# Kernel optimization log

Hardware: AMD Instinct MI355X
Metric: run time of the kernel (lower is better)

Reference implementation:

```python
import jax, jax.numpy as jnp
import numpy as np

DIM = 1024
NUM_HEADS = 16
HD = DIM // NUM_HEADS  # 64
ROPE_DIM = 64
ROPE_BASE = 10000.0


def setup_inputs() -> dict:
    key = jax.random.key(0)
    ks = jax.random.split(key, 5)
    B, N = 2, 2048
    s = 0.02
    return {
        "x": jax.random.normal(ks[0], (B, N, DIM), dtype=jnp.float32),
        "qkv_w": jax.random.normal(ks[1], (3 * DIM, DIM), dtype=jnp.float32) * s,
        "qkv_b": jax.random.normal(ks[2], (3 * DIM,), dtype=jnp.float32) * s,
        "proj_w": jax.random.normal(ks[3], (DIM, DIM), dtype=jnp.float32) * s,
        "proj_b": jax.random.normal(ks[4], (DIM,), dtype=jnp.float32) * s,
    }


def _apply_rope(t):
    # t: [B, H, N, D] with D even; interleaved (even, odd) pair rotation
    D = t.shape[-1]
    N = t.shape[2]
    pos = jnp.arange(N, dtype=t.dtype)
    inv = 1.0 / (ROPE_BASE ** (jnp.arange(0, D, 2, dtype=t.dtype) / D))
    freqs = pos[:, None] * inv[None, :]          # [N, D/2]
    cos = jnp.cos(freqs)[None, None]             # [1,1,N,D/2]
    sin = jnp.sin(freqs)[None, None]
    e = t[..., 0::2]
    o = t[..., 1::2]
    eo = e * cos - o * sin
    oo = e * sin + o * cos
    return jnp.stack([eo, oo], axis=-1).reshape(t.shape)


def reference(x, qkv_w, qkv_b, proj_w, proj_b):
    B, N, C = x.shape
    H, D = NUM_HEADS, HD
    scale = D ** -0.5
    qkv = x @ qkv_w.T + qkv_b                     # [B,N,3C]
    qkv = qkv.reshape(B, N, 3, H, D).transpose(2, 0, 3, 1, 4)  # [3,B,H,N,D]
    q, k, v = qkv[0], qkv[1], qkv[2]
    # RoPE on first ROPE_DIM dims of each head (here ROPE_DIM == HD)
    q = jnp.concatenate([_apply_rope(q[..., :ROPE_DIM]), q[..., ROPE_DIM:]], axis=-1)
    k = jnp.concatenate([_apply_rope(k[..., :ROPE_DIM]), k[..., ROPE_DIM:]], axis=-1)
    attn = jnp.einsum('bhnd,bhmd->bhnm', q, k) * scale
    attn = jax.nn.softmax(attn, axis=-1)
    out = jnp.einsum('bhnm,bhmd->bhnd', attn, v)  # [B,H,N,D]
    out = out.transpose(0, 2, 1, 3).reshape(B, N, C)
    return out @ proj_w.T + proj_b
```

## Files before the change

### kernel.cpp

```cpp
#include <hip/hip_runtime.h>
#include <hip/hip_bf16.h>
#include <stdint.h>

#define DIM   1024
#define NH    16
#define HDIM  64
#define SEQ   2048
#define BATCH 2
#define BHN   32
#define MTOK  4096
#define SC2   0.18033688f

using u16 = unsigned short;
using u32 = unsigned int;
typedef __attribute__((ext_vector_type(8))) short short8;
typedef __attribute__((ext_vector_type(4))) float f32x4;
typedef __attribute__((ext_vector_type(16))) float f32x16;

__device__ __forceinline__ u16 f2bf(float f) {
  __hip_bfloat16 h = __float2bfloat16(f);
  return *reinterpret_cast<u16*>(&h);
}
__device__ __forceinline__ u32 pk2(float lo, float hi) {
  return (u32)f2bf(lo) | ((u32)f2bf(hi) << 16);
}
__device__ __forceinline__ u32 cvtpk(float lo, float hi) {
  u32 r;
  asm("v_cvt_pk_bf16_f32 %0, %1, %2" : "=v"(r) : "v"(lo), "v"(hi));
  return r;
}

__device__ __forceinline__ void gload16(const void* g, void* lds) {
  __builtin_amdgcn_global_load_lds(
      (const __attribute__((address_space(1))) u32*)g,
      (__attribute__((address_space(3))) u32*)lds, 16, 0, 0);
}

#define PREP_A 1048576
#define PREP_B 1835008
#define PREP_C 2097152
#define PREP_E 2162688
__global__ void k_prep(const float4* __restrict__ x, const float4* __restrict__ qw,
                       const float4* __restrict__ pw, ushort4* __restrict__ xb,
                       ushort4* __restrict__ qwb, ushort4* __restrict__ pwb,
                       float2* __restrict__ tab) {
  int i = blockIdx.x * blockDim.x + threadIdx.x;
  if (i < PREP_A) {
    float4 v = x[i];
    xb[i] = make_ushort4(f2bf(v.x), f2bf(v.y), f2bf(v.z), f2bf(v.w));
  } else if (i < PREP_B) {
    int j = i - PREP_A;
    float4 v = qw[j];
    qwb[j] = make_ushort4(f2bf(v.x), f2bf(v.y), f2bf(v.z), f2bf(v.w));
  } else if (i < PREP_C) {
    int j = i - PREP_B;
    float4 v = pw[j];
    pwb[j] = make_ushort4(f2bf(v.x), f2bf(v.y), f2bf(v.z), f2bf(v.w));
  } else if (i < PREP_E) {
    int j = i - PREP_C;
    int n = j >> 5, f = j & 31;
    float inv = powf(10000.f, -(2.f * f) / 64.f);
    float s, c;
    sincosf((float)n * inv, &s, &c);
    tab[j] = make_float2(c, s);
  }
}

template <int EPI>
__global__ __launch_bounds__(256, 2) void k_gemm(
    const u16* __restrict__ A, const u16* __restrict__ Bt,
    const float* __restrict__ bias, int K,
    float* __restrict__ out_f, u16* __restrict__ qb, u16* __restrict__ kb,
    u16* __restrict__ vtb, const float2* __restrict__ tab) {
  __shared__ u16 As[128 * 64];
  __shared__ u16 Bs[128 * 64];
  const int tid = threadIdx.x;
  const int wid = tid >> 6, lane = tid & 63;
  const int lq = lane & 15, g = lane >> 4;
  const int wr = wid >> 1, wc = wid & 1;
  const int brow = blockIdx.y * 128;
  const int bcol = blockIdx.x * 128;
  f32x4 acc[4][4] = {};
  const u16* Ab = A + (size_t)brow * K;
  const u16* Bb = Bt + (size_t)bcol * K;

  for (int k0 = 0; k0 < K; k0 += 64) {
#pragma unroll
    for (int t = 0; t < 4; t++) {
      int rl = wid * 32 + t * 8 + (lane >> 3);
      int cs = (lane & 7) ^ (rl & 7);
      gload16(Ab + (size_t)rl * K + k0 + cs * 8, &As[(wid * 32 + t * 8) * 64]);
      gload16(Bb + (size_t)rl * K + k0 + cs * 8, &Bs[(wid * 32 + t * 8) * 64]);
    }
    __syncthreads();
#pragma unroll
    for (int kc = 0; kc < 2; kc++) {
      short8 af[4], bfr[4];
#pragma unroll
      for (int mt = 0; mt < 4; mt++) {
        int r = wr * 64 + mt * 16 + lq;
        af[mt] = *reinterpret_cast<const short8*>(&As[r * 64 + (((kc * 4 + g) ^ (r & 7)) * 8)]);
      }
#pragma unroll
      for (int nt = 0; nt < 4; nt++) {
        int r = wc * 64 + nt * 16 + lq;
        bfr[nt] = *reinterpret_cast<const short8*>(&Bs[r * 64 + (((kc * 4 + g) ^ (r & 7)) * 8)]);
      }
#pragma unroll
      for (int mt = 0; mt < 4; mt++)
#pragma unroll
        for (int nt = 0; nt < 4; nt++)
          acc[mt][nt] = __builtin_amdgcn_mfma_f32_16x16x32_bf16(af[mt], bfr[nt], acc[mt][nt], 0, 0, 0);
    }
    __syncthreads();
  }

#pragma unroll
  for (int mt = 0; mt < 4; mt++) {
    int row0 = brow + wr * 64 + mt * 16 + g * 4;
#pragma unroll
    for (int nt = 0; nt < 4; nt++) {
      int col = bcol + wc * 64 + nt * 16 + lq;
      float bv = bias[col];
      float v[4];
#pragma unroll
      for (int r = 0; r < 4; r++) v[r] = acc[mt][nt][r] + bv;
      if (EPI == 0) {
#pragma unroll
        for (int r = 0; r < 4; r++) out_f[(size_t)(row0 + r) * DIM + col] = v[r];
      } else {
        int which = col >> 10, hd = col & 1023, hdh = hd >> 6, d = hd & 63;
        int bb = row0 >> 11, n0 = row0 & 2047;
        int bh = bb * NH + hdh;
        if (which == 2) {
          uint2 pv = make_uint2(pk2(v[0], v[1]), pk2(v[2], v[3]));
          size_t idx = ((((size_t)bh * 32 + (n0 >> 6)) * 8 + ((n0 >> 3) & 7)) * 64 + d) * 8 + (n0 & 7);
          *reinterpret_cast<uint2*>(&vtb[idx]) = pv;
        } else {
#pragma unroll
          for (int r = 0; r < 4; r++) {
            int n = n0 + r;
            float p = __shfl_xor(v[r], 1);
            float2 cs = tab[n * 32 + (d >> 1)];
            float vv = (d & 1) ? fmaf(p, cs.y, v[r] * cs.x)
                               : fmaf(-p, cs.y, v[r] * cs.x);
            u16 xo = f2bf(vv);
            if (which == 0) {
              qb[((size_t)bh * SEQ + n) * HDIM + d] = xo;
            } else {
              size_t idx = ((((size_t)bh * 32 + (n >> 6)) * 8 + (d >> 3)) * 64 + (n & 63)) * 8 + (d & 7);
              kb[idx] = xo;
            }
          }
        }
      }
    }
  }
}

__global__ __launch_bounds__(256, 2) void k_attn(
    const u16* __restrict__ qg, const u16* __restrict__ kg,
    const u16* __restrict__ vg, u16* __restrict__ aout) {
  __shared__ __align__(16) char smem[49152];
  const int tid = threadIdx.x;
  const int wid = tid >> 6, lane = tid & 63;
  const int l31 = lane & 31, h = lane >> 5;

  const int bid = blockIdx.x;
  const int xcd = bid & 7, slot = bid >> 3;
  const int bh = xcd * 4 + (slot >> 4);
  const int qt = slot & 15;
  const int b = bh >> 4, hh = bh & 15;
  const int q0 = qt * 128 + wid * 32;

  const u16* kbase = kg + (size_t)bh * SEQ * HDIM;
  const u16* vbase = vg + (size_t)bh * SEQ * HDIM;

  const u16* qrow = qg + ((size_t)bh * SEQ + q0 + l31) * HDIM;
  short8 qf[4];
#pragma unroll
  for (int c = 0; c < 4; c++)
    qf[c] = *reinterpret_cast<const short8*>(qrow + c * 16 + h * 8);

  int koff[4];
#pragma unroll
  for (int c = 0; c < 4; c++)
    koff[c] = (2 * c + h) * 1024 + l31 * 16;

  f32x16 oA = {}, oB = {};
  float m = -INFINITY, lsum = 0.f;

  auto stage = [&](int buf, int tidx) {
    char* kd = smem + buf * 16384;
    const u16* kt = kbase + (size_t)tidx * 4096 + lane * 8;
    const u16* vt = vbase + (size_t)tidx * 4096 + lane * 8;
#pragma unroll
    for (int i = 0; i < 2; i++) {
      int g = wid + i * 4;
      gload16(kt + g * 512, kd + g * 1024);
      gload16(vt + g * 512, kd + 8192 + g * 1024);
    }
  };

  stage(0, 0);
  stage(1, 1);

  const int NT = SEQ / 64;
  int cur = 0, nxt = 2;
  for (int t = 0; t < NT; ++t) {
    if (t < NT - 1) asm volatile("s_waitcnt vmcnt(4)" ::: "memory");
    else            asm volatile("s_waitcnt vmcnt(0)" ::: "memory");
    __builtin_amdgcn_s_barrier();

    const char* kbp = smem + cur * 16384;
    const char* vbp = kbp + 8192;

    f32x16 s0 = {}, s1 = {};
    __builtin_amdgcn_s_setprio(1);
#pragma unroll
    for (int c = 0; c < 4; c++) {
      short8 k0 = *reinterpret_cast<const short8*>(kbp + koff[c]);
      short8 k1 = *reinterpret_cast<const short8*>(kbp + koff[c] + 512);
      s0 = __builtin_amdgcn_mfma_f32_32x32x16_bf16(k0, qf[c], s0, 0, 0, 0);
      s1 = __builtin_amdgcn_mfma_f32_32x32x16_bf16(k1, qf[c], s1, 0, 0, 0);
    }
    __builtin_amdgcn_s_setprio(0);

    short8 vf0[4], vf1[4];
#pragma unroll
    for (int c = 0; c < 4; c++) {
      vf0[c] = *reinterpret_cast<const short8*>(vbp + koff[c]);
      vf1[c] = *reinterpret_cast<const short8*>(vbp + koff[c] + 512);
    }

    if (t + 2 < NT) stage(nxt, t + 2);

    float tm[8];
#pragma unroll
    for (int r = 0; r < 8; r++)
      tm[r] = fmaxf(fmaxf(s0[r], s1[r]), fmaxf(s0[r + 8], s1[r + 8]));
    float ta = fmaxf(fmaxf(tm[0], tm[1]), tm[2]);
    float tb = fmaxf(fmaxf(tm[3], tm[4]), tm[5]);
    float tc = fmaxf(tm[6], tm[7]);
    float tmax = fmaxf(fmaxf(ta, tb), tc);
    tmax = fmaxf(tmax, __shfl_xor(tmax, 32));

    float alpha = 1.f;
    if (__any(tmax - m > 61.0f)) {
      float mnew = fmaxf(m, tmax);
      alpha = exp2f((m - mnew) * SC2);
      m = mnew;
#pragma unroll
      for (int r = 0; r < 16; r++) { oA[r] *= alpha; oB[r] *= alpha; }
    }
    const float nms = -m * SC2;
#pragma unroll
    for (int r = 0; r < 16; r++) s0[r] = exp2f(fmaf(s0[r], SC2, nms));
#pragma unroll
    for (int r = 0; r < 16; r++) s1[r] = exp2f(fmaf(s1[r], SC2, nms));
    float pa = 0.f, pb = 0.f, pc = 0.f, pd = 0.f;
#pragma unroll
    for (int r = 0; r < 4; r++) {
      pa += s0[r] + s0[r + 4];
      pb += s0[r + 8] + s0[r + 12];
      pc += s1[r] + s1[r + 4];
      pd += s1[r + 8] + s1[r + 12];
    }
    float psum = (pa + pb) + (pc + pd);
    psum += __shfl_xor(psum, 32);
    lsum = lsum * alpha + psum;

    short8 pf[4];
    {
      union { u32 u[4]; short8 v; } pp;
      u32 a0, a1, b0, b1;
      a0 = cvtpk(s0[0], s0[1]);  a1 = cvtpk(s0[2], s0[3]);
      b0 = cvtpk(s0[4], s0[5]);  b1 = cvtpk(s0[6], s0[7]);
      { auto r0 = __builtin_amdgcn_permlane32_swap(a0, b0, false, false);
        auto r1 = __builtin_amdgcn_permlane32_swap(a1, b1, false, false);
        pp.u[0] = r0[0]; pp.u[1] = r1[0]; pp.u[2] = r0[1]; pp.u[3] = r1[1]; pf[0] = pp.v; }
      a0 = cvtpk(s0[8], s0[9]);   a1 = cvtpk(s0[10], s0[11]);
      b0 = cvtpk(s0[12], s0[13]); b1 = cvtpk(s0[14], s0[15]);
      { auto r0 = __builtin_amdgcn_permlane32_swap(a0, b0, false, false);
        auto r1 = __builtin_amdgcn_permlane32_swap(a1, b1, false, false);
        pp.u[0] = r0[0]; pp.u[1] = r1[0]; pp.u[2] = r0[1]; pp.u[3] = r1[1]; pf[1] = pp.v; }
      a0 = cvtpk(s1[0], s1[1]);  a1 = cvtpk(s1[2], s1[3]);
      b0 = cvtpk(s1[4], s1[5]);  b1 = cvtpk(s1[6], s1[7]);
      { auto r0 = __builtin_amdgcn_permlane32_swap(a0, b0, false, false);
        auto r1 = __builtin_amdgcn_permlane32_swap(a1, b1, false, false);
        pp.u[0] = r0[0]; pp.u[1] = r1[0]; pp.u[2] = r0[1]; pp.u[3] = r1[1]; pf[2] = pp.v; }
      a0 = cvtpk(s1[8], s1[9]);   a1 = cvtpk(s1[10], s1[11]);
      b0 = cvtpk(s1[12], s1[13]); b1 = cvtpk(s1[14], s1[15]);
      { auto r0 = __builtin_amdgcn_permlane32_swap(a0, b0, false, false);
        auto r1 = __builtin_amdgcn_permlane32_swap(a1, b1, false, false);
        pp.u[0] = r0[0]; pp.u[1] = r1[0]; pp.u[2] = r0[1]; pp.u[3] = r1[1]; pf[3] = pp.v; }
    }

    __builtin_amdgcn_s_setprio(1);
#pragma unroll
    for (int c = 0; c < 4; c++) {
      oA = __builtin_amdgcn_mfma_f32_32x32x16_bf16(vf0[c], pf[c], oA, 0, 0, 0);
      oB = __builtin_amdgcn_mfma_f32_32x32x16_bf16(vf1[c], pf[c], oB, 0, 0, 0);
    }
    __builtin_amdgcn_s_setprio(0);

    cur = cur == 2 ? 0 : cur + 1;
    nxt = nxt == 2 ? 0 : nxt + 1;
  }

  float invl = 1.0f / lsum;
  int n = q0 + l31;
  u16* op = aout + ((size_t)(b * SEQ + n)) * DIM + hh * HDIM;
#pragma unroll
  for (int g = 0; g < 4; g++) {
    u32 w0 = pk2(oA[4 * g] * invl, oA[4 * g + 1] * invl);
    u32 w1 = pk2(oA[4 * g + 2] * invl, oA[4 * g + 3] * invl);
    *reinterpret_cast<uint2*>(op + 8 * g + 4 * h) = make_uint2(w0, w1);
    u32 x0 = pk2(oB[4 * g] * invl, oB[4 * g + 1] * invl);
    u32 x1 = pk2(oB[4 * g + 2] * invl, oB[4 * g + 3] * invl);
    *reinterpret_cast<uint2*>(op + 32 + 8 * g + 4 * h) = make_uint2(x0, x1);
  }
}

extern "C" void kernel_launch(void* const* d_in, const int* in_sizes, int n_in,
                              void* d_out, int out_size, void* d_ws, size_t ws_size,
                              hipStream_t stream) {
  (void)in_sizes; (void)n_in; (void)out_size; (void)ws_size;
  const float* x      = (const float*)d_in[0];
  const float* qkv_w  = (const float*)d_in[1];
  const float* qkv_b  = (const float*)d_in[2];
  const float* proj_w = (const float*)d_in[3];
  const float* proj_b = (const float*)d_in[4];
  float* out = (float*)d_out;

  char* w = (char*)d_ws;
  u16* xb     = (u16*)w;  w += (size_t)MTOK * DIM * 2;
  u16* wqkvb  = (u16*)w;  w += (size_t)3 * DIM * DIM * 2;
  u16* wprojb = (u16*)w;  w += (size_t)DIM * DIM * 2;
  u16* qb     = (u16*)w;  w += (size_t)BHN * SEQ * HDIM * 2;
  u16* kb     = (u16*)w;  w += (size_t)BHN * SEQ * HDIM * 2;
  u16* vtb    = (u16*)w;  w += (size_t)BHN * SEQ * HDIM * 2;
  u16* aout   = (u16*)w;  w += (size_t)MTOK * DIM * 2;
  float2* tab = (float2*)w;

  k_prep<<<(PREP_E + 255) / 256, 256, 0, stream>>>(
      (const float4*)x, (const float4*)qkv_w, (const float4*)proj_w,
      (ushort4*)xb, (ushort4*)wqkvb, (ushort4*)wprojb, tab);

  k_gemm<1><<<dim3(3 * DIM / 128, MTOK / 128), 256, 0, stream>>>(
      xb, wqkvb, qkv_b, DIM, nullptr, qb, kb, vtb, tab);

  k_attn<<<512, 256, 0, stream>>>(qb, kb, vtb, aout);

  k_gemm<0><<<dim3(DIM / 128, MTOK / 128), 256, 0, stream>>>(
      aout, wprojb, proj_b, DIM, out, nullptr, nullptr, nullptr, nullptr);
}
```

Baseline: 133.7 us.

## Switch attention to 16x16x32 MFMA tiles with LDS-staged P and smaller query blocks

The attention kernel now gives each wave 16 queries instead of 32 and uses 16x16x32 bf16 MFMAs. The K and V^T global layouts in the QKV GEMM epilogue are reordered to match the new fragment shapes. The probability matrix is sent through a per-wave LDS scratch instead of permlane swaps, and the K/V ring drops from triple to double buffering. Along with the higher launch-bounds target and twice as many blocks, this is meant to raise occupancy and parallelism. The cost is an extra barrier per tile, less prefetch depth, and each K/V tile being loaded by twice as many blocks.

```diff
diff --git a/kernel.cpp b/kernel.cpp
--- a/kernel.cpp
+++ b/kernel.cpp
@@ -15,7 +15,6 @@
 using u32 = unsigned int;
 typedef __attribute__((ext_vector_type(8))) short short8;
 typedef __attribute__((ext_vector_type(4))) float f32x4;
-typedef __attribute__((ext_vector_type(16))) float f32x16;
 
 __device__ __forceinline__ u16 f2bf(float f) {
   __hip_bfloat16 h = __float2bfloat16(f);
@@ -134,7 +133,8 @@
         int bh = bb * NH + hdh;
         if (which == 2) {
           uint2 pv = make_uint2(pk2(v[0], v[1]), pk2(v[2], v[3]));
-          size_t idx = ((((size_t)bh * 32 + (n0 >> 6)) * 8 + ((n0 >> 3) & 7)) * 64 + d) * 8 + (n0 & 7);
+          size_t idx = (((size_t)bh * 32 + (n0 >> 6)) * 8 + ((n0 & 63) >> 5) * 4 + (d >> 4)) * 512
+                     + ((n0 >> 3) & 3) * 128 + (d & 15) * 8 + (n0 & 7);
           *reinterpret_cast<uint2*>(&vtb[idx]) = pv;
         } else {
 #pragma unroll
@@ -148,7 +148,8 @@
             if (which == 0) {
               qb[((size_t)bh * SEQ + n) * HDIM + d] = xo;
             } else {
-              size_t idx = ((((size_t)bh * 32 + (n >> 6)) * 8 + (d >> 3)) * 64 + (n & 63)) * 8 + (d & 7);
+              size_t idx = (((size_t)bh * 32 + (n >> 6)) * 8 + ((n & 63) >> 4) * 2 + (d >> 5)) * 512
+                         + ((d >> 3) & 3) * 128 + (n & 15) * 8 + (d & 7);
               kb[idx] = xo;
             }
           }
@@ -158,91 +159,78 @@
   }
 }
 
-__global__ __launch_bounds__(256, 2) void k_attn(
+__global__ __launch_bounds__(256, 4) void k_attn(
     const u16* __restrict__ qg, const u16* __restrict__ kg,
     const u16* __restrict__ vg, u16* __restrict__ aout) {
-  __shared__ __align__(16) char smem[49152];
+  __shared__ __align__(16) char smem[40960];
   const int tid = threadIdx.x;
   const int wid = tid >> 6, lane = tid & 63;
-  const int l31 = lane & 31, h = lane >> 5;
+  const int q = lane & 15, g = lane >> 4;
 
   const int bid = blockIdx.x;
   const int xcd = bid & 7, slot = bid >> 3;
-  const int bh = xcd * 4 + (slot >> 4);
-  const int qt = slot & 15;
+  const int bh = xcd * 4 + (slot >> 5);
+  const int qt = slot & 31;
   const int b = bh >> 4, hh = bh & 15;
-  const int q0 = qt * 128 + wid * 32;
+  const int q0 = qt * 64 + wid * 16;
 
   const u16* kbase = kg + (size_t)bh * SEQ * HDIM;
   const u16* vbase = vg + (size_t)bh * SEQ * HDIM;
 
-  const u16* qrow = qg + ((size_t)bh * SEQ + q0 + l31) * HDIM;
-  short8 qf[4];
-#pragma unroll
-  for (int c = 0; c < 4; c++)
-    qf[c] = *reinterpret_cast<const short8*>(qrow + c * 16 + h * 8);
-
-  int koff[4];
-#pragma unroll
-  for (int c = 0; c < 4; c++)
-    koff[c] = (2 * c + h) * 1024 + l31 * 16;
-
-  f32x16 oA = {}, oB = {};
+  const u16* qrow = qg + ((size_t)bh * SEQ + q0 + q) * HDIM;
+  short8 qf[2];
+  qf[0] = *reinterpret_cast<const short8*>(qrow + g * 8);
+  qf[1] = *reinterpret_cast<const short8*>(qrow + 32 + g * 8);
+
+  u16* Pq = (u16*)(smem + 32768 + wid * 2048) + q * 64;
+
+  f32x4 o0 = {}, o1 = {}, o2 = {}, o3 = {};
   float m = -INFINITY, lsum = 0.f;
 
   auto stage = [&](int buf, int tidx) {
     char* kd = smem + buf * 16384;
     const u16* kt = kbase + (size_t)tidx * 4096 + lane * 8;
     const u16* vt = vbase + (size_t)tidx * 4096 + lane * 8;
-#pragma unroll
-    for (int i = 0; i < 2; i++) {
-      int g = wid + i * 4;
-      gload16(kt + g * 512, kd + g * 1024);
-      gload16(vt + g * 512, kd + 8192 + g * 1024);
-    }
+    gload16(kt + wid * 512,       kd + wid * 1024);
+    gload16(kt + (wid + 4) * 512, kd + (wid + 4) * 1024);
+    gload16(vt + wid * 512,       kd + 8192 + wid * 1024);
+    gload16(vt + (wid + 4) * 512, kd + 8192 + (wid + 4) * 1024);
   };
 
   stage(0, 0);
   stage(1, 1);
 
   const int NT = SEQ / 64;
-  int cur = 0, nxt = 2;
   for (int t = 0; t < NT; ++t) {
     if (t < NT - 1) asm volatile("s_waitcnt vmcnt(4)" ::: "memory");
     else            asm volatile("s_waitcnt vmcnt(0)" ::: "memory");
     __builtin_amdgcn_s_barrier();
 
-    const char* kbp = smem + cur * 16384;
+    const char* kbp = smem + (t & 1) * 16384;
     const char* vbp = kbp + 8192;
 
-    f32x16 s0 = {}, s1 = {};
+    f32x4 sv[4] = {};
     __builtin_amdgcn_s_setprio(1);
 #pragma unroll
-    for (int c = 0; c < 4; c++) {
-      short8 k0 = *reinterpret_cast<const short8*>(kbp + koff[c]);
-      short8 k1 = *reinterpret_cast<const short8*>(kbp + koff[c] + 512);
-      s0 = __builtin_amdgcn_mfma_f32_32x32x16_bf16(k0, qf[c], s0, 0, 0, 0);
-      s1 = __builtin_amdgcn_mfma_f32_32x32x16_bf16(k1, qf[c], s1, 0, 0, 0);
-    }
+    for (int s = 0; s < 4; s++)
+#pragma unroll
+      for (int kc = 0; kc < 2; kc++) {
+        short8 kf = *reinterpret_cast<const short8*>(kbp + (s * 2 + kc) * 1024 + lane * 16);
+        sv[s] = __builtin_amdgcn_mfma_f32_16x16x32_bf16(kf, qf[kc], sv[s], 0, 0, 0);
+      }
     __builtin_amdgcn_s_setprio(0);
 
-    short8 vf0[4], vf1[4];
-#pragma unroll
-    for (int c = 0; c < 4; c++) {
-      vf0[c] = *reinterpret_cast<const short8*>(vbp + koff[c]);
-      vf1[c] = *reinterpret_cast<const short8*>(vbp + koff[c] + 512);
-    }
-
-    if (t + 2 < NT) stage(nxt, t + 2);
-
-    float tm[8];
-#pragma unroll
-    for (int r = 0; r < 8; r++)
-      tm[r] = fmaxf(fmaxf(s0[r], s1[r]), fmaxf(s0[r + 8], s1[r + 8]));
-    float ta = fmaxf(fmaxf(tm[0], tm[1]), tm[2]);
-    float tb = fmaxf(fmaxf(tm[3], tm[4]), tm[5]);
-    float tc = fmaxf(tm[6], tm[7]);
-    float tmax = fmaxf(fmaxf(ta, tb), tc);
+    short8 vfa[4];
+#pragma unroll
+    for (int ds = 0; ds < 4; ds++)
+      vfa[ds] = *reinterpret_cast<const short8*>(vbp + ds * 1024 + lane * 16);
+
+    float mx[4];
+#pragma unroll
+    for (int s = 0; s < 4; s++)
+      mx[s] = fmaxf(fmaxf(sv[s][0], sv[s][1]), fmaxf(sv[s][2], sv[s][3]));
+    float tmax = fmaxf(fmaxf(mx[0], mx[1]), fmaxf(mx[2], mx[3]));
+    tmax = fmaxf(tmax, __shfl_xor(tmax, 16));
     tmax = fmaxf(tmax, __shfl_xor(tmax, 32));
 
     float alpha = 1.f;
@@ -251,75 +239,63 @@
       alpha = exp2f((m - mnew) * SC2);
       m = mnew;
 #pragma unroll
-      for (int r = 0; r < 16; r++) { oA[r] *= alpha; oB[r] *= alpha; }
+      for (int r = 0; r < 4; r++) { o0[r] *= alpha; o1[r] *= alpha; o2[r] *= alpha; o3[r] *= alpha; }
     }
     const float nms = -m * SC2;
 #pragma unroll
-    for (int r = 0; r < 16; r++) s0[r] = exp2f(fmaf(s0[r], SC2, nms));
-#pragma unroll
-    for (int r = 0; r < 16; r++) s1[r] = exp2f(fmaf(s1[r], SC2, nms));
-    float pa = 0.f, pb = 0.f, pc = 0.f, pd = 0.f;
-#pragma unroll
-    for (int r = 0; r < 4; r++) {
-      pa += s0[r] + s0[r + 4];
-      pb += s0[r + 8] + s0[r + 12];
-      pc += s1[r] + s1[r + 4];
-      pd += s1[r + 8] + s1[r + 12];
-    }
-    float psum = (pa + pb) + (pc + pd);
+    for (int s = 0; s < 4; s++)
+#pragma unroll
+      for (int r = 0; r < 4; r++) sv[s][r] = exp2f(fmaf(sv[s][r], SC2, nms));
+    float p01 = (sv[0][0] + sv[0][1]) + (sv[0][2] + sv[0][3]);
+    float p23 = (sv[1][0] + sv[1][1]) + (sv[1][2] + sv[1][3]);
+    float p45 = (sv[2][0] + sv[2][1]) + (sv[2][2] + sv[2][3]);
+    float p67 = (sv[3][0] + sv[3][1]) + (sv[3][2] + sv[3][3]);
+    float psum = (p01 + p23) + (p45 + p67);
+    psum += __shfl_xor(psum, 16);
     psum += __shfl_xor(psum, 32);
     lsum = lsum * alpha + psum;
 
-    short8 pf[4];
+#pragma unroll
+    for (int s = 0; s < 4; s++) {
+      uint2 w = make_uint2(cvtpk(sv[s][0], sv[s][1]), cvtpk(sv[s][2], sv[s][3]));
+      *reinterpret_cast<uint2*>(Pq + s * 16 + g * 4) = w;
+    }
+    short8 pf0 = *reinterpret_cast<const short8*>(Pq + g * 8);
+    short8 pf1 = *reinterpret_cast<const short8*>(Pq + 32 + g * 8);
+
+    __builtin_amdgcn_s_setprio(1);
+    o0 = __builtin_amdgcn_mfma_f32_16x16x32_bf16(vfa[0], pf0, o0, 0, 0, 0);
+    o1 = __builtin_amdgcn_mfma_f32_16x16x32_bf16(vfa[1], pf0, o1, 0, 0, 0);
+    o2 = __builtin_amdgcn_mfma_f32_16x16x32_bf16(vfa[2], pf0, o2, 0, 0, 0);
+    o3 = __builtin_amdgcn_mfma_f32_16x16x32_bf16(vfa[3], pf0, o3, 0, 0, 0);
     {
-      union { u32 u[4]; short8 v; } pp;
-      u32 a0, a1, b0, b1;
-      a0 = cvtpk(s0[0], s0[1]);  a1 = cvtpk(s0[2], s0[3]);
-      b0 = cvtpk(s0[4], s0[5]);  b1 = cvtpk(s0[6], s0[7]);
-      { auto r0 = __builtin_amdgcn_permlane32_swap(a0, b0, false, false);
-        auto r1 = __builtin_amdgcn_permlane32_swap(a1, b1, false, false);
-        pp.u[0] = r0[0]; pp.u[1] = r1[0]; pp.u[2] = r0[1]; pp.u[3] = r1[1]; pf[0] = pp.v; }
-      a0 = cvtpk(s0[8], s0[9]);   a1 = cvtpk(s0[10], s0[11]);
-      b0 = cvtpk(s0[12], s0[13]); b1 = cvtpk(s0[14], s0[15]);
-      { auto r0 = __builtin_amdgcn_permlane32_swap(a0, b0, false, false);
-        auto r1 = __builtin_amdgcn_permlane32_swap(a1, b1, false, false);
-        pp.u[0] = r0[0]; pp.u[1] = r1[0]; pp.u[2] = r0[1]; pp.u[3] = r1[1]; pf[1] = pp.v; }
-      a0 = cvtpk(s1[0], s1[1]);  a1 = cvtpk(s1[2], s1[3]);
-      b0 = cvtpk(s1[4], s1[5]);  b1 = cvtpk(s1[6], s1[7]);
-      { auto r0 = __builtin_amdgcn_permlane32_swap(a0, b0, false, false);
-        auto r1 = __builtin_amdgcn_permlane32_swap(a1, b1, false, false);
-        pp.u[0] = r0[0]; pp.u[1] = r1[0]; pp.u[2] = r0[1]; pp.u[3] = r1[1]; pf[2] = pp.v; }
-      a0 = cvtpk(s1[8], s1[9]);   a1 = cvtpk(s1[10], s1[11]);
-      b0 = cvtpk(s1[12], s1[13]); b1 = cvtpk(s1[14], s1[15]);
-      { auto r0 = __builtin_amdgcn_permlane32_swap(a0, b0, false, false);
-        auto r1 = __builtin_amdgcn_permlane32_swap(a1, b1, false, false);
-        pp.u[0] = r0[0]; pp.u[1] = r1[0]; pp.u[2] = r0[1]; pp.u[3] = r1[1]; pf[3] = pp.v; }
-    }
-
-    __builtin_amdgcn_s_setprio(1);
-#pragma unroll
-    for (int c = 0; c < 4; c++) {
-      oA = __builtin_amdgcn_mfma_f32_32x32x16_bf16(vf0[c], pf[c], oA, 0, 0, 0);
-      oB = __builtin_amdgcn_mfma_f32_32x32x16_bf16(vf1[c], pf[c], oB, 0, 0, 0);
+      short8 v4 = *reinterpret_cast<const short8*>(vbp + 4 * 1024 + lane * 16);
+      short8 v5 = *reinterpret_cast<const short8*>(vbp + 5 * 1024 + lane * 16);
+      short8 v6 = *reinterpret_cast<const short8*>(vbp + 6 * 1024 + lane * 16);
+      short8 v7 = *reinterpret_cast<const short8*>(vbp + 7 * 1024 + lane * 16);
+      o0 = __builtin_amdgcn_mfma_f32_16x16x32_bf16(v4, pf1, o0, 0, 0, 0);
+      o1 = __builtin_amdgcn_mfma_f32_16x16x32_bf16(v5, pf1, o1, 0, 0, 0);
+      o2 = __builtin_amdgcn_mfma_f32_16x16x32_bf16(v6, pf1, o2, 0, 0, 0);
+      o3 = __builtin_amdgcn_mfma_f32_16x16x32_bf16(v7, pf1, o3, 0, 0, 0);
     }
     __builtin_amdgcn_s_setprio(0);
 
-    cur = cur == 2 ? 0 : cur + 1;
-    nxt = nxt == 2 ? 0 : nxt + 1;
+    asm volatile("s_waitcnt lgkmcnt(0)" ::: "memory");
+    __builtin_amdgcn_s_barrier();
+    if (t + 2 < NT) stage(t & 1, t + 2);
   }
 
   float invl = 1.0f / lsum;
-  int n = q0 + l31;
+  int n = q0 + q;
   u16* op = aout + ((size_t)(b * SEQ + n)) * DIM + hh * HDIM;
-#pragma unroll
-  for (int g = 0; g < 4; g++) {
-    u32 w0 = pk2(oA[4 * g] * invl, oA[4 * g + 1] * invl);
-    u32 w1 = pk2(oA[4 * g + 2] * invl, oA[4 * g + 3] * invl);
-    *reinterpret_cast<uint2*>(op + 8 * g + 4 * h) = make_uint2(w0, w1);
-    u32 x0 = pk2(oB[4 * g] * invl, oB[4 * g + 1] * invl);
-    u32 x1 = pk2(oB[4 * g + 2] * invl, oB[4 * g + 3] * invl);
-    *reinterpret_cast<uint2*>(op + 32 + 8 * g + 4 * h) = make_uint2(x0, x1);
-  }
+  *reinterpret_cast<uint2*>(op + 0  + 4 * g) =
+      make_uint2(pk2(o0[0] * invl, o0[1] * invl), pk2(o0[2] * invl, o0[3] * invl));
+  *reinterpret_cast<uint2*>(op + 16 + 4 * g) =
+      make_uint2(pk2(o1[0] * invl, o1[1] * invl), pk2(o1[2] * invl, o1[3] * invl));
+  *reinterpret_cast<uint2*>(op + 32 + 4 * g) =
+      make_uint2(pk2(o2[0] * invl, o2[1] * invl), pk2(o2[2] * invl, o2[3] * invl));
+  *reinterpret_cast<uint2*>(op + 48 + 4 * g) =
+      make_uint2(pk2(o3[0] * invl, o3[1] * invl), pk2(o3[2] * invl, o3[3] * invl));
 }
 
 extern "C" void kernel_launch(void* const* d_in, const int* in_sizes, int n_in,
@@ -350,7 +326,7 @@
   k_gemm<1><<<dim3(3 * DIM / 128, MTOK / 128), 256, 0, stream>>>(
       xb, wqkvb, qkv_b, DIM, nullptr, qb, kb, vtb, tab);
 
-  k_attn<<<512, 256, 0, stream>>>(qb, kb, vtb, aout);
+  k_attn<<<1024, 256, 0, stream>>>(qb, kb, vtb, aout);
 
   k_gemm<0><<<dim3(DIM / 128, MTOK / 128), 256, 0, stream>>>(
       aout, wprojb, proj_b, DIM, out, nullptr, nullptr, nullptr, nullptr);
```

Measured after the change: 183.4 us. +37.1%, slower.
